# Performance work log

Measured on AMD Instinct MI355X. Metric: run time of the kernel, lower is better.

## Reference

```python
import jax, jax.numpy as jnp
import numpy as np

EPS = 1e-5  # nn.BatchNorm2d default eps
C1, C2 = 256, 256
B, C, H, W = 8, 512, 48, 48
G = 4                 # len(sizes)
CG = C // G           # per-stage out channels (in_channels // group)
OUT = 512             # out_channels


def setup_inputs() -> dict:
    key = jax.random.key(0)
    ks = jax.random.split(key, 16)
    rn = lambda k, shape, s=0.05: jax.random.normal(k, shape, jnp.float32) * s
    return {
        "feats":   jax.random.normal(ks[0], (B, C, H, W), jnp.float32),
        # per-stage 1x1-conv params, stacked over the G=4 pyramid stages
        "theta_w": rn(ks[1], (G, C1, C)),
        "theta_b": rn(ks[2], (G, C1)),
        "phi_w":   rn(ks[3], (G, C1, C)),
        "phi_b":   rn(ks[4], (G, C1)),
        "g_w":     rn(ks[5], (G, C2, C)),
        "g_b":     rn(ks[6], (G, C2)),
        "w_w":     rn(ks[7], (G, CG, C2)),
        "w_b":     rn(ks[8], (G, CG)),
        "w_gamma": 1.0 + rn(ks[9],  (G, CG)),
        "w_beta":  rn(ks[10], (G, CG)),
        # bottleneck_concat: Conv2d(2C -> OUT, 1x1) + BatchNorm2d(OUT)
        "bc_w":     rn(ks[11], (OUT, 2 * C)),
        "bc_b":     rn(ks[12], (OUT,)),
        "bc_gamma": 1.0 + rn(ks[13], (OUT,)),
        "bc_beta":  rn(ks[14], (OUT,)),
    }


def _bn(x, gamma, beta):
    # x: (B, C, N); training-mode BatchNorm2d over (batch, spatial)
    mean = x.mean(axis=(0, 2), keepdims=True)
    var = x.var(axis=(0, 2), keepdims=True)
    return (x - mean) * jax.lax.rsqrt(var + EPS) * gamma[None, :, None] + beta[None, :, None]


def _stage(xf, tw, tb, pw, pb, gw, gb, ww, wb, gamma, beta):
    # xf: (B, C, N). One MS_NONLocalBlock2D (scale=1, dot_product) stage.
    th = jnp.einsum('oc,bcn->bon', tw, xf) + tb[None, :, None]   # (B, c1, N)
    ph = jnp.einsum('oc,bcn->bon', pw, xf) + pb[None, :, None]   # (B, c1, N)
    gx = jnp.einsum('oc,bcn->bon', gw, xf) + gb[None, :, None]   # (B, c2, N)
    f = jnp.einsum('bcm,bcn->bmn', th, ph) * (tw.shape[0] ** -0.5)  # theta^T phi, scaled by c1^-0.5
    a = jax.nn.softmax(f, axis=-1)
    y = jnp.einsum('bmn,bcn->bcm', a, gx)                         # (B, c2, N)
    wy = jnp.einsum('oc,bcn->bon', ww, y) + wb[None, :, None]     # W conv 1x1: (B, CG, N)
    return _bn(wy, gamma, beta)


def reference(feats, theta_w, theta_b, phi_w, phi_b, g_w, g_b, w_w, w_b,
              w_gamma, w_beta, bc_w, bc_b, bc_gamma, bc_beta):
    b, c, h, w = feats.shape
    n = h * w
    xf = feats.reshape(b, c, n)
    priors = jax.vmap(_stage, in_axes=(None,) + (0,) * 10)(
        xf, theta_w, theta_b, phi_w, phi_b, g_w, g_b, w_w, w_b, w_gamma, w_beta
    )  # (G, B, CG, N)
    # concat order in torch: [feats, p0, p1, p2, p3] along channels
    pr = jnp.transpose(priors, (1, 0, 2, 3)).reshape(b, c, n)
    ctx = jnp.concatenate([xf, pr], axis=1)  # (B, 2C, N)
    out = jnp.einsum('oc,bcn->bon', bc_w, ctx) + bc_b[None, :, None]
    out = _bn(out, bc_gamma, bc_beta)  # dropout=0 -> identity
    return out.reshape(b, bc_w.shape[0], h, w)
```

## Files before the change

kernel.cpp:

```cpp
#include <hip/hip_runtime.h>
#include <hip/hip_bf16.h>

#define EPS 1e-5f
#define Bn 8
#define Cn 512
#define Nn 2304
#define C1n 256
#define C2n 256
#define CGn 128

typedef __bf16 bf16_t;
typedef __bf16 bf16x8 __attribute__((ext_vector_type(8)));
typedef float f32x4 __attribute__((ext_vector_type(4)));

#define MFMA16(a, b, c) __builtin_amdgcn_mfma_f32_16x16x32_bf16(a, b, c, 0, 0, 0)

__device__ __forceinline__ void gload16(const bf16_t* g, const bf16_t* l) {
  __builtin_amdgcn_global_load_lds(
      (const __attribute__((address_space(1))) void*)g,
      (__attribute__((address_space(3))) void*)l, 16, 0, 0);
}

static constexpr size_t P_TW = 0;
static constexpr size_t P_TB = 524288;
static constexpr size_t P_PW = 525312;
static constexpr size_t P_PB = 1049600;
static constexpr size_t P_GW = 1050624;
static constexpr size_t P_GB = 1574912;
static constexpr size_t P_WW = 1575936;
static constexpr size_t P_WB = 1707008;
static constexpr size_t P_WG = 1707520;
static constexpr size_t P_WBE = 1708032;
static constexpr size_t P_BCW = 1708544;
static constexpr size_t P_BCB = 2232832;
static constexpr size_t P_BCG = 2233344;
static constexpr size_t P_BCBE = 2233856;

static constexpr size_t OFF_WPAR  = 0;
static constexpr size_t OFF_BIASF = 4468736;
static constexpr size_t OFF_SW    = 4470784;
static constexpr size_t OFF_TW2   = 4472832;
static constexpr size_t OFF_SO    = 4474880;
static constexpr size_t OFF_TO    = 4476928;
static constexpr size_t OFF_STATW = 4478976;
static constexpr size_t OFF_STATO = 4487168;
static constexpr size_t OFF_ARENA = 4495360;
static constexpr size_t QS  = 589824;
static constexpr size_t SL2 = 2 * QS;
static constexpr size_t OVL_BCWF = OFF_ARENA;
static constexpr size_t OVL_UN   = OFF_ARENA + 2097152;
static constexpr size_t OFF_XBFT_IN_OUT = 18874368;

struct WArgs {
  const float* src[14];
  unsigned n[14];
  unsigned off[14];
};

__global__ __launch_bounds__(256) void k_wconv(WArgs a, bf16_t* __restrict__ par) {
  int which = blockIdx.y;
  const float* s = a.src[which];
  unsigned n = a.n[which];
  bf16_t* dst = par + a.off[which];
  size_t stride = (size_t)gridDim.x * blockDim.x;
  for (size_t i = (size_t)blockIdx.x * blockDim.x + threadIdx.x; i < n; i += stride)
    dst[i] = (bf16_t)s[i];
}

__global__ __launch_bounds__(256) void k_xpose(const float* __restrict__ feats,
                                               bf16_t* __restrict__ xbfT) {
  __shared__ bf16_t tile[64][72];
  int b = blockIdx.z, c0 = blockIdx.y * 64, n0 = blockIdx.x * 64;
  int tid = threadIdx.x;
  int cl = tid >> 4, nl4 = (tid & 15) * 4;
#pragma unroll
  for (int e = 0; e < 4; e++) {
    int c = e * 16 + cl;
    float4 v = *(const float4*)(feats + ((size_t)b * Cn + c0 + c) * Nn + n0 + nl4);
    tile[nl4 + 0][c] = (bf16_t)v.x;
    tile[nl4 + 1][c] = (bf16_t)v.y;
    tile[nl4 + 2][c] = (bf16_t)v.z;
    tile[nl4 + 3][c] = (bf16_t)v.w;
  }
  __syncthreads();
  int r = tid >> 2, ch = tid & 3;
#pragma unroll
  for (int e = 0; e < 2; e++) {
    int cc = (ch + e * 4) * 8;
    bf16x8 v = *(const bf16x8*)(&tile[r][cc]);
    *(bf16x8*)(xbfT + ((size_t)b * Nn + n0 + r) * Cn + c0 + cc) = v;
  }
}

__global__ __launch_bounds__(256) void k_projKV(
    const bf16_t* __restrict__ xbfT, const bf16_t* __restrict__ par,
    bf16_t* __restrict__ arena) {
  __shared__ alignas(16) bf16_t xsT[64][40];
  int z = blockIdx.z, s = z >> 1, p = z & 1;
  int g = s >> 3, b = s & 7;
  int tid = threadIdx.x, w = tid >> 6, lane = tid & 63;
  int l15 = lane & 15, quad = lane >> 4;
  int srow = tid >> 2, sch = (tid & 3) * 8;
  int n0 = blockIdx.x * 64;
  const bf16_t* xsrc = xbfT + ((size_t)b * Nn + n0 + srow) * Cn + sch;

  if (p == 0) {
    const bf16_t* W = par + P_PW + (size_t)g * C1n * Cn;
    const bf16_t* bias = par + P_PB + g * C1n;
    bf16_t* out = arena + (size_t)s * SL2;
    int o0 = blockIdx.y * 64;
    f32x4 acc[4];
#pragma unroll
    for (int j = 0; j < 4; j++) acc[j] = (f32x4){0.f, 0.f, 0.f, 0.f};
    for (int kk = 0; kk < 16; kk++) {
      int c0 = kk * 32;
      __syncthreads();
      *(bf16x8*)(&xsT[srow][sch]) = *(const bf16x8*)(xsrc + c0);
      __syncthreads();
      bf16x8 a = *(const bf16x8*)(&xsT[w * 16 + l15][quad * 8]);
#pragma unroll
      for (int j = 0; j < 4; j++) {
        bf16x8 bw = *(const bf16x8*)(W + (size_t)(o0 + j * 16 + l15) * Cn + c0 + quad * 8);
        acc[j] = MFMA16(a, bw, acc[j]);
      }
    }
#pragma unroll
    for (int j = 0; j < 4; j++) {
      int col = o0 + j * 16 + l15;
      int chk = col >> 3, ci = col & 7;
      float bv = (float)bias[col];
#pragma unroll
      for (int r = 0; r < 4; r++) {
        int row = n0 + w * 16 + quad * 4 + r;
        out[(size_t)row * C1n + ((chk ^ (row & 7)) << 3) + ci] = (bf16_t)(acc[j][r] + bv);
      }
    }
  } else {
    const bf16_t* W = par + P_GW + (size_t)g * C2n * Cn;
    const bf16_t* bias = par + P_GB + g * C2n;
    bf16_t* out = arena + (size_t)s * SL2 + QS;
    int c20 = blockIdx.y * 64 + w * 16;
    f32x4 acc[4];
#pragma unroll
    for (int j = 0; j < 4; j++) acc[j] = (f32x4){0.f, 0.f, 0.f, 0.f};
    for (int kk = 0; kk < 16; kk++) {
      int c0 = kk * 32;
      __syncthreads();
      *(bf16x8*)(&xsT[srow][sch]) = *(const bf16x8*)(xsrc + c0);
      __syncthreads();
      bf16x8 a = *(const bf16x8*)(W + (size_t)(c20 + l15) * Cn + c0 + quad * 8);
#pragma unroll
      for (int j = 0; j < 4; j++) {
        bf16x8 bx = *(const bf16x8*)(&xsT[j * 16 + l15][quad * 8]);
        acc[j] = MFMA16(a, bx, acc[j]);
      }
    }
#pragma unroll
    for (int r = 0; r < 4; r++) {
      int row = c20 + quad * 4 + r;
      float bv = (float)bias[row];
#pragma unroll
      for (int j = 0; j < 4; j++)
        out[(size_t)row * Nn + n0 + j * 16 + l15] = (bf16_t)(acc[j][r] + bv);
    }
  }
}

__global__ __launch_bounds__(256, 2) void k_attn_wy(
    const float* __restrict__ feats, const bf16_t* __restrict__ arena,
    const bf16_t* __restrict__ par, bf16_t* __restrict__ wyOut) {
  __shared__ alignas(16) bf16_t sh[32768 + 5120];

  int mblk = blockIdx.x, gb = blockIdx.y;
  int g = gb >> 3, b = gb & 7;
  const bf16_t* Kp = arena + (size_t)gb * SL2;
  const bf16_t* Vp = Kp + QS;

  int tid = threadIdx.x, w = tid >> 6, lane = tid & 63;
  int l15 = lane & 15, quad = lane >> 4;
  int m0 = mblk * 128;
  int mw0 = m0 + w * 32;
  int w64 = w << 6;
  bf16_t* pw = sh + 32768 + w * 1280;

  bf16x8 qf[16];
  {
    bf16_t* xs = sh + 24576 + w * 1280;
    const bf16_t* Wt = par + P_TW + (size_t)g * C1n * Cn;
    const bf16_t* tb = par + P_TB + g * C1n;
    f32x4 qacc[2][16];
#pragma unroll
    for (int rt = 0; rt < 2; rt++)
#pragma unroll
      for (int ot = 0; ot < 16; ot++) qacc[rt][ot] = (f32x4){0.f, 0.f, 0.f, 0.f};

    for (int kc = 0; kc < 16; kc++) {
#pragma unroll
      for (int ps = 0; ps < 4; ps++) {
        int idx = ps * 64 + lane;
        int cc = idx >> 3;
        int nn = (idx & 7) * 4;
        const float4 v =
            *(const float4*)(feats + ((size_t)b * Cn + kc * 32 + cc) * Nn + mw0 + nn);
        xs[(nn + 0) * 40 + cc] = (bf16_t)v.x;
        xs[(nn + 1) * 40 + cc] = (bf16_t)v.y;
        xs[(nn + 2) * 40 + cc] = (bf16_t)v.z;
        xs[(nn + 3) * 40 + cc] = (bf16_t)v.w;
      }
#pragma unroll
      for (int rt = 0; rt < 2; rt++) {
        bf16x8 a = *(const bf16x8*)(xs + (rt * 16 + l15) * 40 + quad * 8);
#pragma unroll
        for (int ot = 0; ot < 16; ot++) {
          bf16x8 bw = *(const bf16x8*)(Wt + (size_t)(ot * 16 + l15) * Cn + kc * 32 + quad * 8);
          qacc[rt][ot] = MFMA16(a, bw, qacc[rt][ot]);
        }
      }
    }
#pragma unroll
    for (int rt = 0; rt < 2; rt++)
#pragma unroll
      for (int kc8 = 0; kc8 < 8; kc8++) {
#pragma unroll
        for (int h = 0; h < 2; h++) {
          int ot = kc8 * 2 + h;
          float bv = (float)tb[ot * 16 + l15];
#pragma unroll
          for (int r = 0; r < 4; r++)
            pw[(quad * 4 + r) * 40 + h * 16 + l15] = (bf16_t)(qacc[rt][ot][r] + bv);
        }
        qf[rt * 8 + kc8] = *(const bf16x8*)(pw + l15 * 40 + quad * 8);
      }
  }

  f32x4 oacc[2][16];
#pragma unroll
  for (int rt = 0; rt < 2; rt++)
#pragma unroll
    for (int ct = 0; ct < 16; ct++) oacc[rt][ct] = (f32x4){0.f, 0.f, 0.f, 0.f};
  f32x4 lacc[2];
  lacc[0] = (f32x4){0.f, 0.f, 0.f, 0.f};
  lacc[1] = (f32x4){0.f, 0.f, 0.f, 0.f};

  bf16x8 ones;
#pragma unroll
  for (int i = 0; i < 8; i++) ones[i] = (bf16_t)1.0f;
  const float SC = 0.0625f * 1.44269504088896f;

#pragma unroll
  for (int e = 0; e < 4; e++) {
    int cid = e * 256 + tid;
    gload16(Kp + (size_t)(cid >> 5) * C1n + ((cid & 31) << 3),
            sh + ((e << 8) + w64) * 8);
    gload16(Vp + (size_t)(cid >> 2) * Nn + ((((cid & 3) ^ ((cid >> 3) & 3))) << 3),
            sh + 16384 + ((e << 8) + w64) * 8);
  }
  __syncthreads();

  int cur = 0;
  int xrk = l15 & 7;
  int xrv = (l15 >> 1) & 3;
  for (int t = 0; t < 72; t++) {
    if (t < 71) {
      int nn0 = (t + 1) * 32;
      bf16_t* kd = sh + (cur ^ 1) * 8192;
      bf16_t* vd = sh + 16384 + (cur ^ 1) * 8192;
#pragma unroll
      for (int e = 0; e < 4; e++) {
        int cid = e * 256 + tid;
        gload16(Kp + (size_t)(nn0 + (cid >> 5)) * C1n + ((cid & 31) << 3),
                kd + ((e << 8) + w64) * 8);
        gload16(Vp + (size_t)(cid >> 2) * Nn + nn0 + ((((cid & 3) ^ ((cid >> 3) & 3))) << 3),
                vd + ((e << 8) + w64) * 8);
      }
    }
    const bf16_t* kbuf = sh + cur * 8192;
    const bf16_t* vbuf = sh + 16384 + cur * 8192;

    f32x4 sacc[2][2];
#pragma unroll
    for (int rt = 0; rt < 2; rt++)
#pragma unroll
      for (int nt = 0; nt < 2; nt++) sacc[rt][nt] = (f32x4){0.f, 0.f, 0.f, 0.f};
    __builtin_amdgcn_s_setprio(1);
#pragma unroll
    for (int ks = 0; ks < 8; ks++) {
#pragma unroll
      for (int nt = 0; nt < 2; nt++) {
        bf16x8 kb = *(const bf16x8*)(kbuf + (nt * 16 + l15) * 256 +
                                     (((ks * 4 + quad) ^ xrk) << 3));
        sacc[0][nt] = MFMA16(qf[ks], kb, sacc[0][nt]);
        sacc[1][nt] = MFMA16(qf[8 + ks], kb, sacc[1][nt]);
      }
    }
    __builtin_amdgcn_s_setprio(0);
#pragma unroll
    for (int rt = 0; rt < 2; rt++)
#pragma unroll
      for (int nt = 0; nt < 2; nt++)
#pragma unroll
        for (int r = 0; r < 4; r++)
          pw[(rt * 16 + quad * 4 + r) * 40 + nt * 16 + l15] =
              (bf16_t)exp2f(sacc[rt][nt][r] * SC);
    bf16x8 pa0 = *(const bf16x8*)(pw + l15 * 40 + quad * 8);
    bf16x8 pa1 = *(const bf16x8*)(pw + (16 + l15) * 40 + quad * 8);
    lacc[0] = MFMA16(pa0, ones, lacc[0]);
    lacc[1] = MFMA16(pa1, ones, lacc[1]);
    __builtin_amdgcn_s_setprio(1);
#pragma unroll
    for (int ct = 0; ct < 16; ct++) {
      bf16x8 vb = *(const bf16x8*)(vbuf + (ct * 16 + l15) * 32 +
                                   ((quad ^ xrv) << 3));
      oacc[0][ct] = MFMA16(pa0, vb, oacc[0][ct]);
      oacc[1][ct] = MFMA16(pa1, vb, oacc[1][ct]);
    }
    __builtin_amdgcn_s_setprio(0);
    __syncthreads();
    cur ^= 1;
  }

  float inv[2][4];
#pragma unroll
  for (int rt = 0; rt < 2; rt++)
#pragma unroll
    for (int r = 0; r < 4; r++) inv[rt][r] = 1.f / lacc[rt][r];

  const bf16_t* Wg = par + P_WW + (size_t)g * CGn * C2n;
  const bf16_t* wbias = par + P_WB + g * CGn;
#pragma unroll
  for (int rt = 0; rt < 2; rt++) {
    bf16x8 yf[8];
#pragma unroll
    for (int kc8 = 0; kc8 < 8; kc8++) {
#pragma unroll
      for (int h = 0; h < 2; h++) {
        int ct = kc8 * 2 + h;
#pragma unroll
        for (int r = 0; r < 4; r++)
          pw[(quad * 4 + r) * 40 + h * 16 + l15] = (bf16_t)(oacc[rt][ct][r] * inv[rt][r]);
      }
      yf[kc8] = *(const bf16x8*)(pw + l15 * 40 + quad * 8);
    }
#pragma unroll
    for (int ot = 0; ot < 8; ot++) {
      f32x4 wyacc = (f32x4){0.f, 0.f, 0.f, 0.f};
#pragma unroll
      for (int ks = 0; ks < 8; ks++) {
        bf16x8 wv = *(const bf16x8*)(Wg + (size_t)(ot * 16 + l15) * C2n + ks * 32 + quad * 8);
        wyacc = MFMA16(yf[ks], wv, wyacc);
      }
      int o = ot * 16 + l15;
      float bv = (float)wbias[o];
#pragma unroll
      for (int r = 0; r < 4; r++)
        wyOut[((size_t)b * Nn + mw0 + rt * 16 + quad * 4 + r) * 512 + g * 128 + o] =
            (bf16_t)(wyacc[r] + bv);
    }
  }
}

__global__ __launch_bounds__(256) void k_wy_stats(const bf16_t* __restrict__ wyBF,
                                                  double* __restrict__ stats) {
  __shared__ float sred[1024];
  int b = blockIdx.y, m0 = blockIdx.x * 64, tid = threadIdx.x;
  for (int i = tid; i < 1024; i += 256) sred[i] = 0.f;
  __syncthreads();
  int ch8 = (tid & 63) * 8, r0 = tid >> 6;
  float s[8], q[8];
#pragma unroll
  for (int j = 0; j < 8; j++) { s[j] = 0.f; q[j] = 0.f; }
  for (int k = 0; k < 16; k++) {
    int row = k * 4 + r0;
    bf16x8 v = *(const bf16x8*)(wyBF + ((size_t)b * Nn + m0 + row) * 512 + ch8);
#pragma unroll
    for (int j = 0; j < 8; j++) {
      float f = (float)v[j];
      s[j] += f;
      q[j] += f * f;
    }
  }
#pragma unroll
  for (int j = 0; j < 8; j++) {
    atomicAdd(&sred[ch8 + j], s[j]);
    atomicAdd(&sred[512 + ch8 + j], q[j]);
  }
  __syncthreads();
  for (int i = tid; i < 1024; i += 256) atomicAdd(&stats[i], (double)sred[i]);
}

__global__ void k_bn_st(const double* __restrict__ stats, const bf16_t* __restrict__ gamma,
                        const bf16_t* __restrict__ beta, float* __restrict__ sArr,
                        float* __restrict__ tArr, double inv_count) {
  int ch = threadIdx.x;
  double mean = stats[ch] * inv_count;
  double var = stats[512 + ch] * inv_count - mean * mean;
  double s = (double)(float)gamma[ch] / sqrt(var + (double)EPS);
  sArr[ch] = (float)s;
  tArr[ch] = (float)((double)(float)beta[ch] - mean * s);
}

__global__ __launch_bounds__(256) void k_fold(
    const bf16_t* __restrict__ par, const float* __restrict__ sW,
    const float* __restrict__ tW, bf16_t* __restrict__ bcwF, float* __restrict__ biasF) {
  int oo = blockIdx.x;
  int tid = threadIdx.x;
  const bf16_t* row = par + P_BCW + (size_t)oo * 1024;
  bf16_t* orow = bcwF + (size_t)oo * 1024;
  float part = 0.f;
  for (int c = tid; c < 512; c += 256) orow[c] = row[c];
  for (int c = 512 + tid; c < 1024; c += 256) {
    float wv = (float)row[c];
    orow[c] = (bf16_t)(wv * sW[c - 512]);
    part += wv * tW[c - 512];
  }
  __shared__ float red[256];
  red[tid] = part;
  __syncthreads();
  for (int s = 128; s > 0; s >>= 1) {
    if (tid < s) red[tid] += red[tid + s];
    __syncthreads();
  }
  if (tid == 0) biasF[oo] = (float)par[P_BCB + oo] + red[0];
}

__global__ __launch_bounds__(256) void k_final(
    const bf16_t* __restrict__ xbfT, const bf16_t* __restrict__ wyBF,
    const bf16_t* __restrict__ bcwF, const float* __restrict__ biasF,
    double* __restrict__ stats, float* __restrict__ un) {
  __shared__ alignas(16) bf16_t xsT[64][40];
  int b = blockIdx.z;
  int tid = threadIdx.x, w = tid >> 6, lane = tid & 63;
  int l15 = lane & 15, quad = lane >> 4;
  int oo0 = blockIdx.y * 64 + w * 16;
  int n0 = blockIdx.x * 64;
  int srow = tid >> 2, sch = (tid & 3) * 8;
  const bf16_t* xsrc = xbfT + ((size_t)b * Nn + n0 + srow) * Cn + sch;

  f32x4 acc[4];
#pragma unroll
  for (int j = 0; j < 4; j++) acc[j] = (f32x4){0.f, 0.f, 0.f, 0.f};

  for (int kk = 0; kk < 16; kk++) {
    int c0 = kk * 32;
    __syncthreads();
    *(bf16x8*)(&xsT[srow][sch]) = *(const bf16x8*)(xsrc + c0);
    __syncthreads();
    bf16x8 a = *(const bf16x8*)(bcwF + (size_t)(oo0 + l15) * 1024 + c0 + quad * 8);
#pragma unroll
    for (int j = 0; j < 4; j++) {
      bf16x8 bx = *(const bf16x8*)(&xsT[j * 16 + l15][quad * 8]);
      acc[j] = MFMA16(a, bx, acc[j]);
    }
  }
  for (int kk = 0; kk < 16; kk++) {
    int c0 = kk * 32 + quad * 8;
    bf16x8 a = *(const bf16x8*)(bcwF + (size_t)(oo0 + l15) * 1024 + 512 + c0);
#pragma unroll
    for (int j = 0; j < 4; j++) {
      bf16x8 bw = *(const bf16x8*)(wyBF + ((size_t)b * Nn + n0 + j * 16 + l15) * 512 + c0);
      acc[j] = MFMA16(a, bw, acc[j]);
    }
  }

#pragma unroll
  for (int r = 0; r < 4; r++) {
    int row = oo0 + quad * 4 + r;
    float bv = biasF[row];
    float s = 0.f, q = 0.f;
#pragma unroll
    for (int j = 0; j < 4; j++) {
      float v = acc[j][r] + bv;
      un[((size_t)b * 512 + row) * Nn + n0 + j * 16 + l15] = v;
      s += v;
      q += v * v;
    }
    s += __shfl_xor(s, 1); q += __shfl_xor(q, 1);
    s += __shfl_xor(s, 2); q += __shfl_xor(q, 2);
    s += __shfl_xor(s, 4); q += __shfl_xor(q, 4);
    s += __shfl_xor(s, 8); q += __shfl_xor(q, 8);
    if (l15 == 0) {
      atomicAdd(&stats[row], (double)s);
      atomicAdd(&stats[512 + row], (double)q);
    }
  }
}

__global__ __launch_bounds__(256) void k_norm(const float4* __restrict__ un,
                                              const float* __restrict__ sO,
                                              const float* __restrict__ tO,
                                              float4* __restrict__ out) {
  size_t i = (size_t)blockIdx.x * 256 + threadIdx.x;
  if (i >= (size_t)2359296) return;
  size_t r = i / 576;
  int ch = (int)(r & 511);
  float sc = sO[ch], tc = tO[ch];
  float4 v = un[i];
  float4 o;
  o.x = v.x * sc + tc;
  o.y = v.y * sc + tc;
  o.z = v.z * sc + tc;
  o.w = v.w * sc + tc;
  out[i] = o;
}

extern "C" void kernel_launch(void* const* d_in, const int* in_sizes, int n_in,
                              void* d_out, int out_size, void* d_ws, size_t ws_size,
                              hipStream_t stream) {
  const float* feats = (const float*)d_in[0];

  char* ws = (char*)d_ws;
  bf16_t* WPAR = (bf16_t*)(ws + OFF_WPAR);
  float* biasF = (float*)(ws + OFF_BIASF);
  float* sW = (float*)(ws + OFF_SW);
  float* tW = (float*)(ws + OFF_TW2);
  float* sO = (float*)(ws + OFF_SO);
  float* tO = (float*)(ws + OFF_TO);
  double* statsWy = (double*)(ws + OFF_STATW);
  double* statsO = (double*)(ws + OFF_STATO);
  bf16_t* arena = (bf16_t*)(ws + OFF_ARENA);
  bf16_t* bcwF = (bf16_t*)(ws + OVL_BCWF);
  float* unScr = (float*)(ws + OVL_UN);
  bf16_t* wyScr = (bf16_t*)d_out;
  bf16_t* xbfT = (bf16_t*)((char*)d_out + OFF_XBFT_IN_OUT);

  static const unsigned par_off[14] = {
      (unsigned)P_TW, (unsigned)P_TB, (unsigned)P_PW, (unsigned)P_PB,
      (unsigned)P_GW, (unsigned)P_GB, (unsigned)P_WW, (unsigned)P_WB,
      (unsigned)P_WG, (unsigned)P_WBE, (unsigned)P_BCW, (unsigned)P_BCB,
      (unsigned)P_BCG, (unsigned)P_BCBE};
  WArgs wa;
  for (int i = 0; i < 14; i++) {
    wa.src[i] = (const float*)d_in[i + 1];
    wa.n[i] = (unsigned)in_sizes[i + 1];
    wa.off[i] = par_off[i];
  }

  hipMemsetAsync(ws + OFF_STATW, 0, 16384, stream);

  k_wconv<<<dim3(256, 14), 256, 0, stream>>>(wa, WPAR);
  k_xpose<<<dim3(36, 8, 8), 256, 0, stream>>>(feats, xbfT);
  k_projKV<<<dim3(36, 4, 64), 256, 0, stream>>>(xbfT, WPAR, arena);
  k_attn_wy<<<dim3(18, 32), 256, 0, stream>>>(feats, arena, WPAR, wyScr);
  k_wy_stats<<<dim3(36, 8), 256, 0, stream>>>(wyScr, statsWy);
  k_bn_st<<<1, 512, 0, stream>>>(statsWy, WPAR + P_WG, WPAR + P_WBE, sW, tW, 1.0 / 18432.0);
  k_fold<<<512, 256, 0, stream>>>(WPAR, sW, tW, bcwF, biasF);
  k_final<<<dim3(36, 8, 8), 256, 0, stream>>>(xbfT, wyScr, bcwF, biasF, statsO, unScr);
  k_bn_st<<<1, 512, 0, stream>>>(statsO, WPAR + P_BCG, WPAR + P_BCBE, sO, tO, 1.0 / 18432.0);
  k_norm<<<9216, 256, 0, stream>>>((const float4*)unScr, sO, tO, (float4*)d_out);
}
```

Before: 861.0 us.

## Split attention work over 8 waves with 16 query rows each

Measured after the change: 1.004 ms. +16.6%, slower.

```diff
diff --git a/kernel.cpp b/kernel.cpp
--- a/kernel.cpp
+++ b/kernel.cpp
@@ -166,7 +166,7 @@
   }
 }
 
-__global__ __launch_bounds__(256, 2) void k_attn_wy(
+__global__ __launch_bounds__(512, 2) void k_attn_wy(
     const float* __restrict__ feats, const bf16_t* __restrict__ arena,
     const bf16_t* __restrict__ par, bf16_t* __restrict__ wyOut) {
   __shared__ alignas(16) bf16_t sh[32768 + 5120];
@@ -179,27 +179,25 @@
   int tid = threadIdx.x, w = tid >> 6, lane = tid & 63;
   int l15 = lane & 15, quad = lane >> 4;
   int m0 = mblk * 128;
-  int mw0 = m0 + w * 32;
+  int mw0 = m0 + w * 16;
   int w64 = w << 6;
-  bf16_t* pw = sh + 32768 + w * 1280;
-
-  bf16x8 qf[16];
+  bf16_t* pw = sh + 32768 + w * 640;
+
+  bf16x8 qf[8];
   {
-    bf16_t* xs = sh + 24576 + w * 1280;
+    bf16_t* xs = sh + 24576 + w * 640;
     const bf16_t* Wt = par + P_TW + (size_t)g * C1n * Cn;
     const bf16_t* tb = par + P_TB + g * C1n;
-    f32x4 qacc[2][16];
-#pragma unroll
-    for (int rt = 0; rt < 2; rt++)
-#pragma unroll
-      for (int ot = 0; ot < 16; ot++) qacc[rt][ot] = (f32x4){0.f, 0.f, 0.f, 0.f};
+    f32x4 qacc[16];
+#pragma unroll
+    for (int ot = 0; ot < 16; ot++) qacc[ot] = (f32x4){0.f, 0.f, 0.f, 0.f};
 
     for (int kc = 0; kc < 16; kc++) {
 #pragma unroll
-      for (int ps = 0; ps < 4; ps++) {
+      for (int ps = 0; ps < 2; ps++) {
         int idx = ps * 64 + lane;
-        int cc = idx >> 3;
-        int nn = (idx & 7) * 4;
+        int cc = idx & 31;
+        int nn = (idx >> 5) * 4;
         const float4 v =
             *(const float4*)(feats + ((size_t)b * Cn + kc * 32 + cc) * Nn + mw0 + nn);
         xs[(nn + 0) * 40 + cc] = (bf16_t)v.x;
@@ -207,40 +205,31 @@
         xs[(nn + 2) * 40 + cc] = (bf16_t)v.z;
         xs[(nn + 3) * 40 + cc] = (bf16_t)v.w;
       }
-#pragma unroll
-      for (int rt = 0; rt < 2; rt++) {
-        bf16x8 a = *(const bf16x8*)(xs + (rt * 16 + l15) * 40 + quad * 8);
-#pragma unroll
-        for (int ot = 0; ot < 16; ot++) {
-          bf16x8 bw = *(const bf16x8*)(Wt + (size_t)(ot * 16 + l15) * Cn + kc * 32 + quad * 8);
-          qacc[rt][ot] = MFMA16(a, bw, qacc[rt][ot]);
-        }
-      }
-    }
-#pragma unroll
-    for (int rt = 0; rt < 2; rt++)
-#pragma unroll
-      for (int kc8 = 0; kc8 < 8; kc8++) {
-#pragma unroll
-        for (int h = 0; h < 2; h++) {
-          int ot = kc8 * 2 + h;
-          float bv = (float)tb[ot * 16 + l15];
-#pragma unroll
-          for (int r = 0; r < 4; r++)
-            pw[(quad * 4 + r) * 40 + h * 16 + l15] = (bf16_t)(qacc[rt][ot][r] + bv);
-        }
-        qf[rt * 8 + kc8] = *(const bf16x8*)(pw + l15 * 40 + quad * 8);
-      }
-  }
-
-  f32x4 oacc[2][16];
-#pragma unroll
-  for (int rt = 0; rt < 2; rt++)
-#pragma unroll
-    for (int ct = 0; ct < 16; ct++) oacc[rt][ct] = (f32x4){0.f, 0.f, 0.f, 0.f};
-  f32x4 lacc[2];
-  lacc[0] = (f32x4){0.f, 0.f, 0.f, 0.f};
-  lacc[1] = (f32x4){0.f, 0.f, 0.f, 0.f};
+      bf16x8 a = *(const bf16x8*)(xs + l15 * 40 + quad * 8);
+#pragma unroll
+      for (int ot = 0; ot < 16; ot++) {
+        bf16x8 bw = *(const bf16x8*)(Wt + (size_t)(ot * 16 + l15) * Cn + kc * 32 + quad * 8);
+        qacc[ot] = MFMA16(a, bw, qacc[ot]);
+      }
+    }
+#pragma unroll
+    for (int kc8 = 0; kc8 < 8; kc8++) {
+#pragma unroll
+      for (int h = 0; h < 2; h++) {
+        int ot = kc8 * 2 + h;
+        float bv = (float)tb[ot * 16 + l15];
+#pragma unroll
+        for (int r = 0; r < 4; r++)
+          pw[(quad * 4 + r) * 40 + h * 16 + l15] = (bf16_t)(qacc[ot][r] + bv);
+      }
+      qf[kc8] = *(const bf16x8*)(pw + l15 * 40 + quad * 8);
+    }
+  }
+
+  f32x4 oacc[16];
+#pragma unroll
+  for (int ct = 0; ct < 16; ct++) oacc[ct] = (f32x4){0.f, 0.f, 0.f, 0.f};
+  f32x4 lacc = (f32x4){0.f, 0.f, 0.f, 0.f};
 
   bf16x8 ones;
 #pragma unroll
@@ -248,12 +237,12 @@
   const float SC = 0.0625f * 1.44269504088896f;
 
 #pragma unroll
-  for (int e = 0; e < 4; e++) {
-    int cid = e * 256 + tid;
+  for (int e = 0; e < 2; e++) {
+    int cid = e * 512 + tid;
     gload16(Kp + (size_t)(cid >> 5) * C1n + ((cid & 31) << 3),
-            sh + ((e << 8) + w64) * 8);
+            sh + ((e << 9) + w64) * 8);
     gload16(Vp + (size_t)(cid >> 2) * Nn + ((((cid & 3) ^ ((cid >> 3) & 3))) << 3),
-            sh + 16384 + ((e << 8) + w64) * 8);
+            sh + 16384 + ((e << 9) + w64) * 8);
   }
   __syncthreads();
 
@@ -266,22 +255,20 @@
       bf16_t* kd = sh + (cur ^ 1) * 8192;
       bf16_t* vd = sh + 16384 + (cur ^ 1) * 8192;
 #pragma unroll
-      for (int e = 0; e < 4; e++) {
-        int cid = e * 256 + tid;
+      for (int e = 0; e < 2; e++) {
+        int cid = e * 512 + tid;
         gload16(Kp + (size_t)(nn0 + (cid >> 5)) * C1n + ((cid & 31) << 3),
-                kd + ((e << 8) + w64) * 8);
+                kd + ((e << 9) + w64) * 8);
         gload16(Vp + (size_t)(cid >> 2) * Nn + nn0 + ((((cid & 3) ^ ((cid >> 3) & 3))) << 3),
-                vd + ((e << 8) + w64) * 8);
+                vd + ((e << 9) + w64) * 8);
       }
     }
     const bf16_t* kbuf = sh + cur * 8192;
     const bf16_t* vbuf = sh + 16384 + cur * 8192;
 
-    f32x4 sacc[2][2];
-#pragma unroll
-    for (int rt = 0; rt < 2; rt++)
-#pragma unroll
-      for (int nt = 0; nt < 2; nt++) sacc[rt][nt] = (f32x4){0.f, 0.f, 0.f, 0.f};
+    f32x4 sacc[2];
+    sacc[0] = (f32x4){0.f, 0.f, 0.f, 0.f};
+    sacc[1] = (f32x4){0.f, 0.f, 0.f, 0.f};
     __builtin_amdgcn_s_setprio(1);
 #pragma unroll
     for (int ks = 0; ks < 8; ks++) {
@@ -289,73 +276,61 @@
       for (int nt = 0; nt < 2; nt++) {
         bf16x8 kb = *(const bf16x8*)(kbuf + (nt * 16 + l15) * 256 +
                                      (((ks * 4 + quad) ^ xrk) << 3));
-        sacc[0][nt] = MFMA16(qf[ks], kb, sacc[0][nt]);
-        sacc[1][nt] = MFMA16(qf[8 + ks], kb, sacc[1][nt]);
+        sacc[nt] = MFMA16(qf[ks], kb, sacc[nt]);
       }
     }
     __builtin_amdgcn_s_setprio(0);
 #pragma unroll
-    for (int rt = 0; rt < 2; rt++)
-#pragma unroll
-      for (int nt = 0; nt < 2; nt++)
-#pragma unroll
-        for (int r = 0; r < 4; r++)
-          pw[(rt * 16 + quad * 4 + r) * 40 + nt * 16 + l15] =
-              (bf16_t)exp2f(sacc[rt][nt][r] * SC);
-    bf16x8 pa0 = *(const bf16x8*)(pw + l15 * 40 + quad * 8);
-    bf16x8 pa1 = *(const bf16x8*)(pw + (16 + l15) * 40 + quad * 8);
-    lacc[0] = MFMA16(pa0, ones, lacc[0]);
-    lacc[1] = MFMA16(pa1, ones, lacc[1]);
+    for (int nt = 0; nt < 2; nt++)
+#pragma unroll
+      for (int r = 0; r < 4; r++)
+        pw[(quad * 4 + r) * 40 + nt * 16 + l15] = (bf16_t)exp2f(sacc[nt][r] * SC);
+    bf16x8 pa = *(const bf16x8*)(pw + l15 * 40 + quad * 8);
+    lacc = MFMA16(pa, ones, lacc);
     __builtin_amdgcn_s_setprio(1);
 #pragma unroll
     for (int ct = 0; ct < 16; ct++) {
       bf16x8 vb = *(const bf16x8*)(vbuf + (ct * 16 + l15) * 32 +
                                    ((quad ^ xrv) << 3));
-      oacc[0][ct] = MFMA16(pa0, vb, oacc[0][ct]);
-      oacc[1][ct] = MFMA16(pa1, vb, oacc[1][ct]);
+      oacc[ct] = MFMA16(pa, vb, oacc[ct]);
     }
     __builtin_amdgcn_s_setprio(0);
     __syncthreads();
     cur ^= 1;
   }
 
-  float inv[2][4];
-#pragma unroll
-  for (int rt = 0; rt < 2; rt++)
-#pragma unroll
-    for (int r = 0; r < 4; r++) inv[rt][r] = 1.f / lacc[rt][r];
+  float inv[4];
+#pragma unroll
+  for (int r = 0; r < 4; r++) inv[r] = 1.f / lacc[r];
 
   const bf16_t* Wg = par + P_WW + (size_t)g * CGn * C2n;
   const bf16_t* wbias = par + P_WB + g * CGn;
-#pragma unroll
-  for (int rt = 0; rt < 2; rt++) {
-    bf16x8 yf[8];
-#pragma unroll
-    for (int kc8 = 0; kc8 < 8; kc8++) {
-#pragma unroll
-      for (int h = 0; h < 2; h++) {
-        int ct = kc8 * 2 + h;
-#pragma unroll
-        for (int r = 0; r < 4; r++)
-          pw[(quad * 4 + r) * 40 + h * 16 + l15] = (bf16_t)(oacc[rt][ct][r] * inv[rt][r]);
-      }
-      yf[kc8] = *(const bf16x8*)(pw + l15 * 40 + quad * 8);
-    }
-#pragma unroll
-    for (int ot = 0; ot < 8; ot++) {
-      f32x4 wyacc = (f32x4){0.f, 0.f, 0.f, 0.f};
-#pragma unroll
-      for (int ks = 0; ks < 8; ks++) {
-        bf16x8 wv = *(const bf16x8*)(Wg + (size_t)(ot * 16 + l15) * C2n + ks * 32 + quad * 8);
-        wyacc = MFMA16(yf[ks], wv, wyacc);
-      }
-      int o = ot * 16 + l15;
-      float bv = (float)wbias[o];
+  bf16x8 yf[8];
+#pragma unroll
+  for (int kc8 = 0; kc8 < 8; kc8++) {
+#pragma unroll
+    for (int h = 0; h < 2; h++) {
+      int ct = kc8 * 2 + h;
 #pragma unroll
       for (int r = 0; r < 4; r++)
-        wyOut[((size_t)b * Nn + mw0 + rt * 16 + quad * 4 + r) * 512 + g * 128 + o] =
-            (bf16_t)(wyacc[r] + bv);
-    }
+        pw[(quad * 4 + r) * 40 + h * 16 + l15] = (bf16_t)(oacc[ct][r] * inv[r]);
+    }
+    yf[kc8] = *(const bf16x8*)(pw + l15 * 40 + quad * 8);
+  }
+#pragma unroll
+  for (int ot = 0; ot < 8; ot++) {
+    f32x4 wyacc = (f32x4){0.f, 0.f, 0.f, 0.f};
+#pragma unroll
+    for (int ks = 0; ks < 8; ks++) {
+      bf16x8 wv = *(const bf16x8*)(Wg + (size_t)(ot * 16 + l15) * C2n + ks * 32 + quad * 8);
+      wyacc = MFMA16(yf[ks], wv, wyacc);
+    }
+    int o = ot * 16 + l15;
+    float bv = (float)wbias[o];
+#pragma unroll
+    for (int r = 0; r < 4; r++)
+      wyOut[((size_t)b * Nn + mw0 + quad * 4 + r) * 512 + g * 128 + o] =
+          (bf16_t)(wyacc[r] + bv);
   }
 }
 
@@ -540,7 +515,7 @@
   k_wconv<<<dim3(256, 14), 256, 0, stream>>>(wa, WPAR);
   k_xpose<<<dim3(36, 8, 8), 256, 0, stream>>>(feats, xbfT);
   k_projKV<<<dim3(36, 4, 64), 256, 0, stream>>>(xbfT, WPAR, arena);
-  k_attn_wy<<<dim3(18, 32), 256, 0, stream>>>(feats, arena, WPAR, wyScr);
+  k_attn_wy<<<dim3(18, 32), 512, 0, stream>>>(feats, arena, WPAR, wyScr);
   k_wy_stats<<<dim3(36, 8), 256, 0, stream>>>(wyScr, statsWy);
   k_bn_st<<<1, 512, 0, stream>>>(statsWy, WPAR + P_WG, WPAR + P_WBE, sW, tW, 1.0 / 18432.0);
   k_fold<<<512, 256, 0, stream>>>(WPAR, sW, tW, bcwF, biasF);
```

## Triple-buffer K/V tiles in attention loop with partial vmcnt waits

Applied to the files above, without the earlier changes.

New measurement: 941.1 us. 9.3% more time.

```diff
diff --git a/kernel.cpp b/kernel.cpp
--- a/kernel.cpp
+++ b/kernel.cpp
@@ -166,10 +166,10 @@
   }
 }
 
-__global__ __launch_bounds__(256, 2) void k_attn_wy(
+__global__ __launch_bounds__(256) void k_attn_wy(
     const float* __restrict__ feats, const bf16_t* __restrict__ arena,
     const bf16_t* __restrict__ par, bf16_t* __restrict__ wyOut) {
-  __shared__ alignas(16) bf16_t sh[32768 + 5120];
+  __shared__ alignas(16) bf16_t sh[54272];
 
   int mblk = blockIdx.x, gb = blockIdx.y;
   int g = gb >> 3, b = gb & 7;
@@ -181,11 +181,11 @@
   int m0 = mblk * 128;
   int mw0 = m0 + w * 32;
   int w64 = w << 6;
-  bf16_t* pw = sh + 32768 + w * 1280;
+  bf16_t* pw = sh + 49152 + w * 1280;
 
   bf16x8 qf[16];
   {
-    bf16_t* xs = sh + 24576 + w * 1280;
+    bf16_t* xs = pw;
     const bf16_t* Wt = par + P_TW + (size_t)g * C1n * Cn;
     const bf16_t* tb = par + P_TB + g * C1n;
     f32x4 qacc[2][16];
@@ -253,18 +253,29 @@
     gload16(Kp + (size_t)(cid >> 5) * C1n + ((cid & 31) << 3),
             sh + ((e << 8) + w64) * 8);
     gload16(Vp + (size_t)(cid >> 2) * Nn + ((((cid & 3) ^ ((cid >> 3) & 3))) << 3),
-            sh + 16384 + ((e << 8) + w64) * 8);
-  }
-  __syncthreads();
-
-  int cur = 0;
+            sh + 24576 + ((e << 8) + w64) * 8);
+  }
+#pragma unroll
+  for (int e = 0; e < 4; e++) {
+    int cid = e * 256 + tid;
+    gload16(Kp + (size_t)(32 + (cid >> 5)) * C1n + ((cid & 31) << 3),
+            sh + 8192 + ((e << 8) + w64) * 8);
+    gload16(Vp + (size_t)(cid >> 2) * Nn + 32 + ((((cid & 3) ^ ((cid >> 3) & 3))) << 3),
+            sh + 24576 + 8192 + ((e << 8) + w64) * 8);
+  }
+  asm volatile("s_waitcnt vmcnt(8)" ::: "memory");
+  __builtin_amdgcn_s_barrier();
+  __builtin_amdgcn_sched_barrier(0);
+
+  int bc = 0;
   int xrk = l15 & 7;
   int xrv = (l15 >> 1) & 3;
   for (int t = 0; t < 72; t++) {
-    if (t < 71) {
-      int nn0 = (t + 1) * 32;
-      bf16_t* kd = sh + (cur ^ 1) * 8192;
-      bf16_t* vd = sh + 16384 + (cur ^ 1) * 8192;
+    if (t < 70) {
+      int nn0 = (t + 2) * 32;
+      int b2 = bc + 2; if (b2 >= 3) b2 -= 3;
+      bf16_t* kd = sh + b2 * 8192;
+      bf16_t* vd = sh + 24576 + b2 * 8192;
 #pragma unroll
       for (int e = 0; e < 4; e++) {
         int cid = e * 256 + tid;
@@ -274,8 +285,8 @@
                 vd + ((e << 8) + w64) * 8);
       }
     }
-    const bf16_t* kbuf = sh + cur * 8192;
-    const bf16_t* vbuf = sh + 16384 + cur * 8192;
+    const bf16_t* kbuf = sh + bc * 8192;
+    const bf16_t* vbuf = sh + 24576 + bc * 8192;
 
     f32x4 sacc[2][2];
 #pragma unroll
@@ -315,8 +326,14 @@
       oacc[1][ct] = MFMA16(pa1, vb, oacc[1][ct]);
     }
     __builtin_amdgcn_s_setprio(0);
-    __syncthreads();
-    cur ^= 1;
+    if (t < 70) {
+      asm volatile("s_waitcnt vmcnt(8)" ::: "memory");
+    } else {
+      asm volatile("s_waitcnt vmcnt(0)" ::: "memory");
+    }
+    __builtin_amdgcn_s_barrier();
+    __builtin_amdgcn_sched_barrier(0);
+    bc = bc + 1; if (bc >= 3) bc -= 3;
   }
 
   float inv[2][4];
```

## Enlarge projection and final GEMM tiles to 128x128 with double-buffered LDS staging

Applied to the files above, without the earlier changes.

Result: faster. 760.8 us (-11.6%).

```diff
diff --git a/kernel.cpp b/kernel.cpp
--- a/kernel.cpp
+++ b/kernel.cpp
@@ -95,74 +95,103 @@
 __global__ __launch_bounds__(256) void k_projKV(
     const bf16_t* __restrict__ xbfT, const bf16_t* __restrict__ par,
     bf16_t* __restrict__ arena) {
-  __shared__ alignas(16) bf16_t xsT[64][40];
+  __shared__ alignas(16) bf16_t xsT[2][5120];
   int z = blockIdx.z, s = z >> 1, p = z & 1;
   int g = s >> 3, b = s & 7;
   int tid = threadIdx.x, w = tid >> 6, lane = tid & 63;
   int l15 = lane & 15, quad = lane >> 4;
-  int srow = tid >> 2, sch = (tid & 3) * 8;
-  int n0 = blockIdx.x * 64;
-  const bf16_t* xsrc = xbfT + ((size_t)b * Nn + n0 + srow) * Cn + sch;
+  int wh = w >> 1, wl = w & 1;
+  int n0 = blockIdx.x * 128;
+  int y0 = blockIdx.y * 128;
+
+  int srow = tid >> 1, sc0 = (tid & 1) * 16;
+  const bf16_t* xrow = xbfT + ((size_t)b * Nn + n0 + srow) * Cn + sc0;
+  bf16_t* st0 = &xsT[0][srow * 40 + sc0];
+  bf16_t* st1 = &xsT[1][srow * 40 + sc0];
+
+  f32x4 acc[4][4];
+#pragma unroll
+  for (int i = 0; i < 4; i++)
+#pragma unroll
+    for (int j = 0; j < 4; j++) acc[i][j] = (f32x4){0.f, 0.f, 0.f, 0.f};
+
+  const bf16_t* W = par + (p == 0 ? P_PW : P_GW) + (size_t)g * 256 * Cn;
+
+  {
+    bf16x8 r0 = *(const bf16x8*)(xrow);
+    bf16x8 r1 = *(const bf16x8*)(xrow + 8);
+    *(bf16x8*)(st0) = r0;
+    *(bf16x8*)(st1 - (st1 - st0)) = r0;
+    *(bf16x8*)(st0 + 8) = r1;
+  }
+  __syncthreads();
+
+  int cur = 0;
+  for (int kk = 0; kk < 16; kk++) {
+    bf16x8 nx0, nx1;
+    if (kk < 15) {
+      nx0 = *(const bf16x8*)(xrow + (kk + 1) * 32);
+      nx1 = *(const bf16x8*)(xrow + (kk + 1) * 32 + 8);
+    }
+    int c0 = kk * 32 + quad * 8;
+    int wbase = y0 + (p == 0 ? wl : wh) * 64;
+    bf16x8 wf[4];
+#pragma unroll
+    for (int j = 0; j < 4; j++)
+      wf[j] = *(const bf16x8*)(W + (size_t)(wbase + j * 16 + l15) * Cn + c0);
+    int xbase = (p == 0 ? wh : wl) * 64;
+    const bf16_t* xb = &xsT[cur][0];
+#pragma unroll
+    for (int i = 0; i < 4; i++) {
+      bf16x8 xf = *(const bf16x8*)(xb + (xbase + i * 16 + l15) * 40 + quad * 8);
+      if (p == 0) {
+#pragma unroll
+        for (int j = 0; j < 4; j++) acc[i][j] = MFMA16(xf, wf[j], acc[i][j]);
+      } else {
+#pragma unroll
+        for (int j = 0; j < 4; j++) acc[j][i] = MFMA16(wf[j], xf, acc[j][i]);
+      }
+    }
+    if (kk < 15) {
+      bf16_t* st = (cur == 0) ? st1 : st0;
+      *(bf16x8*)(st) = nx0;
+      *(bf16x8*)(st + 8) = nx1;
+    }
+    __syncthreads();
+    cur ^= 1;
+  }
 
   if (p == 0) {
-    const bf16_t* W = par + P_PW + (size_t)g * C1n * Cn;
     const bf16_t* bias = par + P_PB + g * C1n;
     bf16_t* out = arena + (size_t)s * SL2;
-    int o0 = blockIdx.y * 64;
-    f32x4 acc[4];
-#pragma unroll
-    for (int j = 0; j < 4; j++) acc[j] = (f32x4){0.f, 0.f, 0.f, 0.f};
-    for (int kk = 0; kk < 16; kk++) {
-      int c0 = kk * 32;
-      __syncthreads();
-      *(bf16x8*)(&xsT[srow][sch]) = *(const bf16x8*)(xsrc + c0);
-      __syncthreads();
-      bf16x8 a = *(const bf16x8*)(&xsT[w * 16 + l15][quad * 8]);
-#pragma unroll
-      for (int j = 0; j < 4; j++) {
-        bf16x8 bw = *(const bf16x8*)(W + (size_t)(o0 + j * 16 + l15) * Cn + c0 + quad * 8);
-        acc[j] = MFMA16(a, bw, acc[j]);
-      }
-    }
 #pragma unroll
     for (int j = 0; j < 4; j++) {
-      int col = o0 + j * 16 + l15;
+      int col = y0 + wl * 64 + j * 16 + l15;
       int chk = col >> 3, ci = col & 7;
       float bv = (float)bias[col];
 #pragma unroll
-      for (int r = 0; r < 4; r++) {
-        int row = n0 + w * 16 + quad * 4 + r;
-        out[(size_t)row * C1n + ((chk ^ (row & 7)) << 3) + ci] = (bf16_t)(acc[j][r] + bv);
-      }
+      for (int i = 0; i < 4; i++)
+#pragma unroll
+        for (int r = 0; r < 4; r++) {
+          int row = n0 + wh * 64 + i * 16 + quad * 4 + r;
+          out[(size_t)row * C1n + ((chk ^ (row & 7)) << 3) + ci] =
+              (bf16_t)(acc[i][j][r] + bv);
+        }
     }
   } else {
-    const bf16_t* W = par + P_GW + (size_t)g * C2n * Cn;
     const bf16_t* bias = par + P_GB + g * C2n;
     bf16_t* out = arena + (size_t)s * SL2 + QS;
-    int c20 = blockIdx.y * 64 + w * 16;
-    f32x4 acc[4];
-#pragma unroll
-    for (int j = 0; j < 4; j++) acc[j] = (f32x4){0.f, 0.f, 0.f, 0.f};
-    for (int kk = 0; kk < 16; kk++) {
-      int c0 = kk * 32;
-      __syncthreads();
-      *(bf16x8*)(&xsT[srow][sch]) = *(const bf16x8*)(xsrc + c0);
-      __syncthreads();
-      bf16x8 a = *(const bf16x8*)(W + (size_t)(c20 + l15) * Cn + c0 + quad * 8);
-#pragma unroll
-      for (int j = 0; j < 4; j++) {
-        bf16x8 bx = *(const bf16x8*)(&xsT[j * 16 + l15][quad * 8]);
-        acc[j] = MFMA16(a, bx, acc[j]);
-      }
-    }
-#pragma unroll
-    for (int r = 0; r < 4; r++) {
-      int row = c20 + quad * 4 + r;
-      float bv = (float)bias[row];
-#pragma unroll
-      for (int j = 0; j < 4; j++)
-        out[(size_t)row * Nn + n0 + j * 16 + l15] = (bf16_t)(acc[j][r] + bv);
-    }
+#pragma unroll
+    for (int j = 0; j < 4; j++)
+#pragma unroll
+      for (int r = 0; r < 4; r++) {
+        int row = y0 + wh * 64 + j * 16 + quad * 4 + r;
+        float bv = (float)bias[row];
+#pragma unroll
+        for (int i = 0; i < 4; i++)
+          out[(size_t)row * Nn + n0 + wl * 64 + i * 16 + l15] =
+              (bf16_t)(acc[j][i][r] + bv);
+      }
   }
 }
 
@@ -427,62 +456,87 @@
     const bf16_t* __restrict__ xbfT, const bf16_t* __restrict__ wyBF,
     const bf16_t* __restrict__ bcwF, const float* __restrict__ biasF,
     double* __restrict__ stats, float* __restrict__ un) {
-  __shared__ alignas(16) bf16_t xsT[64][40];
+  __shared__ alignas(16) bf16_t xsT[2][5120];
   int b = blockIdx.z;
   int tid = threadIdx.x, w = tid >> 6, lane = tid & 63;
   int l15 = lane & 15, quad = lane >> 4;
-  int oo0 = blockIdx.y * 64 + w * 16;
-  int n0 = blockIdx.x * 64;
-  int srow = tid >> 2, sch = (tid & 3) * 8;
-  const bf16_t* xsrc = xbfT + ((size_t)b * Nn + n0 + srow) * Cn + sch;
-
-  f32x4 acc[4];
-#pragma unroll
-  for (int j = 0; j < 4; j++) acc[j] = (f32x4){0.f, 0.f, 0.f, 0.f};
-
-  for (int kk = 0; kk < 16; kk++) {
-    int c0 = kk * 32;
+  int wh = w >> 1, wl = w & 1;
+  int n0 = blockIdx.x * 128;
+  int oo0 = blockIdx.y * 128;
+
+  int srow = tid >> 1, sc0 = (tid & 1) * 16;
+  const bf16_t* xrow = xbfT + ((size_t)b * Nn + n0 + srow) * Cn + sc0;
+  const bf16_t* wrow = wyBF + ((size_t)b * Nn + n0 + srow) * 512 + sc0;
+  bf16_t* stA = &xsT[0][srow * 40 + sc0];
+  bf16_t* stB = &xsT[1][srow * 40 + sc0];
+
+  f32x4 acc[4][4];
+#pragma unroll
+  for (int i = 0; i < 4; i++)
+#pragma unroll
+    for (int j = 0; j < 4; j++) acc[i][j] = (f32x4){0.f, 0.f, 0.f, 0.f};
+
+  {
+    bf16x8 r0 = *(const bf16x8*)(xrow);
+    bf16x8 r1 = *(const bf16x8*)(xrow + 8);
+    *(bf16x8*)(stA) = r0;
+    *(bf16x8*)(stA + 8) = r1;
+  }
+  __syncthreads();
+
+  int cur = 0;
+  for (int kk = 0; kk < 32; kk++) {
+    bf16x8 nx0, nx1;
+    if (kk < 31) {
+      const bf16_t* src = (kk + 1 < 16) ? (xrow + (kk + 1) * 32)
+                                        : (wrow + (kk + 1 - 16) * 32);
+      nx0 = *(const bf16x8*)(src);
+      nx1 = *(const bf16x8*)(src + 8);
+    }
+    int c0 = (kk < 16 ? kk * 32 : 512 + (kk - 16) * 32) + quad * 8;
+    bf16x8 af[4];
+#pragma unroll
+    for (int i = 0; i < 4; i++)
+      af[i] = *(const bf16x8*)(bcwF + (size_t)(oo0 + wh * 64 + i * 16 + l15) * 1024 + c0);
+    const bf16_t* xb = &xsT[cur][0];
+#pragma unroll
+    for (int j = 0; j < 4; j++) {
+      bf16x8 bf = *(const bf16x8*)(xb + (wl * 64 + j * 16 + l15) * 40 + quad * 8);
+#pragma unroll
+      for (int i = 0; i < 4; i++) acc[i][j] = MFMA16(af[i], bf, acc[i][j]);
+    }
+    if (kk < 31) {
+      bf16_t* st = (cur == 0) ? stB : stA;
+      *(bf16x8*)(st) = nx0;
+      *(bf16x8*)(st + 8) = nx1;
+    }
     __syncthreads();
-    *(bf16x8*)(&xsT[srow][sch]) = *(const bf16x8*)(xsrc + c0);
-    __syncthreads();
-    bf16x8 a = *(const bf16x8*)(bcwF + (size_t)(oo0 + l15) * 1024 + c0 + quad * 8);
-#pragma unroll
-    for (int j = 0; j < 4; j++) {
-      bf16x8 bx = *(const bf16x8*)(&xsT[j * 16 + l15][quad * 8]);
-      acc[j] = MFMA16(a, bx, acc[j]);
-    }
-  }
-  for (int kk = 0; kk < 16; kk++) {
-    int c0 = kk * 32 + quad * 8;
-    bf16x8 a = *(const bf16x8*)(bcwF + (size_t)(oo0 + l15) * 1024 + 512 + c0);
-#pragma unroll
-    for (int j = 0; j < 4; j++) {
-      bf16x8 bw = *(const bf16x8*)(wyBF + ((size_t)b * Nn + n0 + j * 16 + l15) * 512 + c0);
-      acc[j] = MFMA16(a, bw, acc[j]);
-    }
-  }
-
-#pragma unroll
-  for (int r = 0; r < 4; r++) {
-    int row = oo0 + quad * 4 + r;
-    float bv = biasF[row];
-    float s = 0.f, q = 0.f;
-#pragma unroll
-    for (int j = 0; j < 4; j++) {
-      float v = acc[j][r] + bv;
-      un[((size_t)b * 512 + row) * Nn + n0 + j * 16 + l15] = v;
-      s += v;
-      q += v * v;
-    }
-    s += __shfl_xor(s, 1); q += __shfl_xor(q, 1);
-    s += __shfl_xor(s, 2); q += __shfl_xor(q, 2);
-    s += __shfl_xor(s, 4); q += __shfl_xor(q, 4);
-    s += __shfl_xor(s, 8); q += __shfl_xor(q, 8);
-    if (l15 == 0) {
-      atomicAdd(&stats[row], (double)s);
-      atomicAdd(&stats[512 + row], (double)q);
-    }
-  }
+    cur ^= 1;
+  }
+
+#pragma unroll
+  for (int i = 0; i < 4; i++)
+#pragma unroll
+    for (int r = 0; r < 4; r++) {
+      int row = oo0 + wh * 64 + i * 16 + quad * 4 + r;
+      float bv = biasF[row];
+      float s = 0.f, q = 0.f;
+#pragma unroll
+      for (int j = 0; j < 4; j++) {
+        float v = acc[i][j][r] + bv;
+        un[((size_t)b * 512 + row) * Nn + n0 + wl * 64 + j * 16 + l15] = v;
+        s += v;
+        q += v * v;
+      }
+      s += __shfl_xor(s, 1); q += __shfl_xor(q, 1);
+      s += __shfl_xor(s, 2); q += __shfl_xor(q, 2);
+      s += __shfl_xor(s, 4); q += __shfl_xor(q, 4);
+      s += __shfl_xor(s, 8); q += __shfl_xor(q, 8);
+      if (l15 == 0) {
+        atomicAdd(&stats[row], (double)s);
+        atomicAdd(&stats[512 + row], (double)q);
+      }
+    }
 }
 
 __global__ __launch_bounds__(256) void k_norm(const float4* __restrict__ un,
@@ -539,12 +593,12 @@
 
   k_wconv<<<dim3(256, 14), 256, 0, stream>>>(wa, WPAR);
   k_xpose<<<dim3(36, 8, 8), 256, 0, stream>>>(feats, xbfT);
-  k_projKV<<<dim3(36, 4, 64), 256, 0, stream>>>(xbfT, WPAR, arena);
+  k_projKV<<<dim3(18, 2, 64), 256, 0, stream>>>(xbfT, WPAR, arena);
   k_attn_wy<<<dim3(18, 32), 256, 0, stream>>>(feats, arena, WPAR, wyScr);
   k_wy_stats<<<dim3(36, 8), 256, 0, stream>>>(wyScr, statsWy);
   k_bn_st<<<1, 512, 0, stream>>>(statsWy, WPAR + P_WG, WPAR + P_WBE, sW, tW, 1.0 / 18432.0);
   k_fold<<<512, 256, 0, stream>>>(WPAR, sW, tW, bcwF, biasF);
-  k_final<<<dim3(36, 8, 8), 256, 0, stream>>>(xbfT, wyScr, bcwF, biasF, statsO, unScr);
+  k_final<<<dim3(18, 4, 8), 256, 0, stream>>>(xbfT, wyScr, bcwF, biasF, statsO, unScr);
   k_bn_st<<<1, 512, 0, stream>>>(statsO, WPAR + P_BCG, WPAR + P_BCBE, sO, tO, 1.0 / 18432.0);
   k_norm<<<9216, 256, 0, stream>>>((const float4*)unScr, sO, tO, (float4*)d_out);
 }
```
